# Optimization experiments

Hardware: AMD Instinct MI355X
Metric: run time of the kernel (lower is better)

The kernel has to match this reference:

```python
import jax, jax.numpy as jnp
import numpy as np

DIM = 128
HEADS = 4
DIM_HEAD = 32
HIDDEN = HEADS * DIM_HEAD  # 128
SCALE = DIM_HEAD ** -0.5


def setup_inputs() -> dict:
    key = jax.random.key(0)
    k1, k2, k3, k4 = jax.random.split(key, 4)
    b, c, h, w = 2, DIM, 64, 64
    x = jax.random.normal(k1, (b, c, h, w), dtype=jnp.float32)
    # conv1x1 weights stored as [out_ch, in_ch] (kernel is 1x1)
    w_qkv = jax.random.normal(k2, (3 * HIDDEN, DIM), dtype=jnp.float32) * (DIM ** -0.5)
    w_out = jax.random.normal(k3, (DIM, HIDDEN), dtype=jnp.float32) * (HIDDEN ** -0.5)
    b_out = jax.random.normal(k4, (DIM,), dtype=jnp.float32) * 0.01
    return {"x": x, "w_qkv": w_qkv, "w_out": w_out, "b_out": b_out}


def reference(x, w_qkv, w_out, b_out):
    b, c, h, w = x.shape
    n = h * w
    xf = x.reshape(b, c, n)                                   # [b,c,n]
    qkv = jnp.einsum('oc,bcn->bon', w_qkv, xf)                # conv1x1, no bias
    q, k, v = jnp.split(qkv, 3, axis=1)                       # each [b,hidden,n]
    q = q.reshape(b, HEADS, DIM_HEAD, n) * SCALE
    k = k.reshape(b, HEADS, DIM_HEAD, n)
    v = v.reshape(b, HEADS, DIM_HEAD, n)
    sim = jnp.einsum('bhdi,bhdj->bhij', q, k)                 # [b,h,n,n]
    attn = jax.nn.softmax(sim, axis=-1)
    out = jnp.einsum('bhij,bhdj->bhdi', attn, v)              # [b,h,d,n]
    out = out.reshape(b, HIDDEN, n)
    out = jnp.einsum('oc,bcn->bon', w_out, out) + b_out[None, :, None]
    return out.reshape(b, c, h, w) + x
```

## Files before the change

### kernel.cpp

```cpp
#include <hip/hip_runtime.h>
#include <hip/hip_bf16.h>

typedef __hip_bfloat16 bf16;
typedef float    f32x16 __attribute__((ext_vector_type(16)));
typedef __bf16   bf16x8 __attribute__((ext_vector_type(8)));
typedef unsigned uint4v __attribute__((ext_vector_type(4)));
typedef int      i32x2  __attribute__((ext_vector_type(2)));

#define N_TOK 4096
#define SCALE_L2E 0.2550348952703927f

__device__ __forceinline__ bf16x8 ld8(const bf16* p) { return *(const bf16x8*)p; }
__device__ __forceinline__ unsigned pack2(float a, float b) {
    unsigned short ua = __builtin_bit_cast(unsigned short, (__bf16)a);
    unsigned short ub = __builtin_bit_cast(unsigned short, (__bf16)b);
    return (unsigned)ua | ((unsigned)ub << 16);
}
__device__ __forceinline__ unsigned short f2b(float f) {
    return __builtin_bit_cast(unsigned short, (__bf16)f);
}
__device__ __forceinline__ __bf16 us2bf(unsigned short u) {
    return __builtin_bit_cast(__bf16, u);
}

__global__ void wconv(const float* __restrict__ wqkv, const float* __restrict__ wout,
                      bf16* __restrict__ wq, bf16* __restrict__ wo) {
    int idx = blockIdx.x * 256 + threadIdx.x;
    if (idx < 384 * 128) {
        float sc = (idx < 128 * 128) ? SCALE_L2E : 1.0f;
        ((unsigned short*)wq)[idx] = f2b(wqkv[idx] * sc);
    } else {
        int j = idx - 384 * 128;
        ((unsigned short*)wo)[j] = f2b(wout[j]);
    }
}

__global__ void __launch_bounds__(256)
qkv_mfma(const float* __restrict__ x, const bf16* __restrict__ wq,
         bf16* __restrict__ qt, bf16* __restrict__ kt, bf16* __restrict__ vt) {
    int tok0 = blockIdx.x * 64;
    int b    = blockIdx.y;
    int z    = blockIdx.z;
    __shared__ unsigned short xs[128 * 64];
    {
        int c = threadIdx.x >> 1, half = threadIdx.x & 1;
        const float4* x4 = (const float4*)(x + (size_t)(b * 128 + c) * N_TOK + tok0 + half * 32);
        unsigned* dst = (unsigned*)&xs[c * 64 + half * 32];
#pragma unroll
        for (int k = 0; k < 8; ++k) {
            float4 v4 = x4[k];
            dst[2 * k]     = pack2(v4.x, v4.y);
            dst[2 * k + 1] = pack2(v4.z, v4.w);
        }
    }
    __syncthreads();
    int lane = threadIdx.x & 63, wv = threadIdx.x >> 6;
    int tc = wv & 1, oh = wv >> 1;
    int ot = z * 2 + oh;
    int o0 = ot * 32;
    int i = lane & 31, hl = lane >> 5;

    bf16x8 xf[8], wf[8];
#pragma unroll
    for (int kb = 0; kb < 8; ++kb) {
        bf16x8 f;
#pragma unroll
        for (int e = 0; e < 8; ++e) f[e] = us2bf(xs[(kb * 16 + hl * 8 + e) * 64 + tc * 32 + i]);
        xf[kb] = f;
        wf[kb] = ld8(wq + (size_t)(o0 + i) * 128 + kb * 16 + hl * 8);
    }

    f32x16 D;
#pragma unroll
    for (int r = 0; r < 16; ++r) D[r] = 0.f;

    if (ot < 8) {
#pragma unroll
        for (int kb = 0; kb < 8; ++kb)
            D = __builtin_amdgcn_mfma_f32_32x32x16_bf16(xf[kb], wf[kb], D, 0, 0, 0);
        bf16* base = (ot < 4) ? qt : kt;
        int h = ot & 3;
        unsigned short* dst = (unsigned short*)(base +
            ((size_t)(b * 4 + h) * N_TOK + tok0 + tc * 32) * 32);
#pragma unroll
        for (int r = 0; r < 16; ++r) {
            int tr = (r & 3) + 8 * (r >> 2) + 4 * hl;
            dst[tr * 32 + i] = f2b(D[r]);
        }
    } else {
#pragma unroll
        for (int kb = 0; kb < 8; ++kb)
            D = __builtin_amdgcn_mfma_f32_32x32x16_bf16(wf[kb], xf[kb], D, 0, 0, 0);
        int h = ot - 8;
        unsigned short* dst = (unsigned short*)(vt +
            (size_t)(b * 4 + h) * (32 * N_TOK) + tok0 + tc * 32);
#pragma unroll
        for (int r = 0; r < 16; ++r) {
            int dr = (r & 3) + 8 * (r >> 2) + 4 * hl;
            dst[(size_t)dr * N_TOK + i] = f2b(D[r]);
        }
    }
}

#define KROW 40
#define KBUF_SZ (128 * KROW * 2)
#define VBUF_OFF (2 * KBUF_SZ)
#define VBUF_SZ (32 * 128 * 2)

__global__ void __launch_bounds__(512)
attn_mfma(const bf16* __restrict__ qt, const bf16* __restrict__ kt,
          const bf16* __restrict__ vt, bf16* __restrict__ ao) {
    int bid = blockIdx.x;
    int bh  = bid & 7;
    int qg  = bid >> 3;
    int tid = threadIdx.x;
    int lane = tid & 63, wv = tid >> 6;
    int qp = wv >> 2;
    int ks = wv & 3;
    int i = lane & 31, hl = lane >> 5;

    __shared__ char lds[2 * KBUF_SZ + 2 * VBUF_SZ];

    const bf16* qb = qt + (size_t)bh * (N_TOK * 32) + (size_t)(qg * 128 + qp * 64) * 32;
    bf16x8 q1a = ld8(qb + i * 32 + hl * 8);
    bf16x8 q2a = ld8(qb + i * 32 + 16 + hl * 8);
    bf16x8 q1b = ld8(qb + (32 + i) * 32 + hl * 8);
    bf16x8 q2b = ld8(qb + (32 + i) * 32 + 16 + hl * 8);

    int u = tid;
    const bf16* ksrc = kt + (size_t)bh * (N_TOK * 32) + (u >> 2) * 32 + (u & 3) * 8;
    const bf16* vsrc = vt + (size_t)bh * (32 * N_TOK) + (size_t)(u >> 4) * N_TOK + (u & 15) * 8;
    int kdst = (u >> 2) * 80 + (u & 3) * 16;
    int vdst = VBUF_OFF + (((u >> 4) * 256 + (u & 15) * 16) ^ (((u >> 4) & 7) << 4));

    int koff1 = (ks * 32 + i) * 80 + hl * 16;
    int koff2 = koff1 + 32;
    int voff1 = VBUF_OFF + ((i * 256 + ks * 64 + hl * 16) ^ ((i & 7) << 4));
    int voff2 = VBUF_OFF + ((i * 256 + ks * 64 + 32 + hl * 16) ^ ((i & 7) << 4));

    f32x16 OA, OB, Z;
#pragma unroll
    for (int r = 0; r < 16; ++r) { OA[r] = 0.f; OB[r] = 0.f; Z[r] = 0.f; }
    float lA = 0.f, lB = 0.f;

    *(uint4v*)(lds + kdst) = *(const uint4v*)ksrc;
    *(uint4v*)(lds + vdst) = *(const uint4v*)vsrc;
    __syncthreads();

    for (int t = 0; t < 32; ++t) {
        int cur = t & 1;
        uint4v nk, nv;
        if (t < 31) {
            nk = *(const uint4v*)(ksrc + (size_t)(t + 1) * 128 * 32);
            nv = *(const uint4v*)(vsrc + (t + 1) * 128);
        }
        bf16x8 ka1 = __builtin_bit_cast(bf16x8, *(const uint4v*)(lds + cur * KBUF_SZ + koff1));
        bf16x8 ka2 = __builtin_bit_cast(bf16x8, *(const uint4v*)(lds + cur * KBUF_SZ + koff2));
        bf16x8 va1 = __builtin_bit_cast(bf16x8, *(const uint4v*)(lds + cur * VBUF_SZ + voff1));
        bf16x8 va2 = __builtin_bit_cast(bf16x8, *(const uint4v*)(lds + cur * VBUF_SZ + voff2));

        f32x16 SA = __builtin_amdgcn_mfma_f32_32x32x16_bf16(ka1, q1a, Z, 0, 0, 0);
        SA = __builtin_amdgcn_mfma_f32_32x32x16_bf16(ka2, q2a, SA, 0, 0, 0);
        f32x16 SB = __builtin_amdgcn_mfma_f32_32x32x16_bf16(ka1, q1b, Z, 0, 0, 0);
        SB = __builtin_amdgcn_mfma_f32_32x32x16_bf16(ka2, q2b, SB, 0, 0, 0);

        float pA[16], pB[16];
#pragma unroll
        for (int r = 0; r < 16; ++r) { pA[r] = __builtin_amdgcn_exp2f(SA[r]); }
#pragma unroll
        for (int r = 0; r < 16; ++r) { pB[r] = __builtin_amdgcn_exp2f(SB[r]); }
#pragma unroll
        for (int r = 0; r < 16; ++r) { lA += pA[r]; lB += pB[r]; }

        {
            unsigned k0 = pack2(pA[0], pA[1]),   k1 = pack2(pA[2], pA[3]);
            unsigned k2 = pack2(pA[4], pA[5]),   k3 = pack2(pA[6], pA[7]);
            unsigned k4 = pack2(pA[8], pA[9]),   k5 = pack2(pA[10], pA[11]);
            unsigned k6 = pack2(pA[12], pA[13]), k7 = pack2(pA[14], pA[15]);
            i32x2 t1 = __builtin_amdgcn_permlane32_swap((int)k0, (int)k2, false, false);
            i32x2 t2 = __builtin_amdgcn_permlane32_swap((int)k1, (int)k3, false, false);
            i32x2 t3 = __builtin_amdgcn_permlane32_swap((int)k4, (int)k6, false, false);
            i32x2 t4 = __builtin_amdgcn_permlane32_swap((int)k5, (int)k7, false, false);
            uint4v B1u = {(unsigned)t1.x, (unsigned)t2.x, (unsigned)t1.y, (unsigned)t2.y};
            uint4v B2u = {(unsigned)t3.x, (unsigned)t4.x, (unsigned)t3.y, (unsigned)t4.y};
            OA = __builtin_amdgcn_mfma_f32_32x32x16_bf16(va1, __builtin_bit_cast(bf16x8, B1u), OA, 0, 0, 0);
            OA = __builtin_amdgcn_mfma_f32_32x32x16_bf16(va2, __builtin_bit_cast(bf16x8, B2u), OA, 0, 0, 0);
        }
        {
            unsigned k0 = pack2(pB[0], pB[1]),   k1 = pack2(pB[2], pB[3]);
            unsigned k2 = pack2(pB[4], pB[5]),   k3 = pack2(pB[6], pB[7]);
            unsigned k4 = pack2(pB[8], pB[9]),   k5 = pack2(pB[10], pB[11]);
            unsigned k6 = pack2(pB[12], pB[13]), k7 = pack2(pB[14], pB[15]);
            i32x2 t1 = __builtin_amdgcn_permlane32_swap((int)k0, (int)k2, false, false);
            i32x2 t2 = __builtin_amdgcn_permlane32_swap((int)k1, (int)k3, false, false);
            i32x2 t3 = __builtin_amdgcn_permlane32_swap((int)k4, (int)k6, false, false);
            i32x2 t4 = __builtin_amdgcn_permlane32_swap((int)k5, (int)k7, false, false);
            uint4v B1u = {(unsigned)t1.x, (unsigned)t2.x, (unsigned)t1.y, (unsigned)t2.y};
            uint4v B2u = {(unsigned)t3.x, (unsigned)t4.x, (unsigned)t3.y, (unsigned)t4.y};
            OB = __builtin_amdgcn_mfma_f32_32x32x16_bf16(va1, __builtin_bit_cast(bf16x8, B1u), OB, 0, 0, 0);
            OB = __builtin_amdgcn_mfma_f32_32x32x16_bf16(va2, __builtin_bit_cast(bf16x8, B2u), OB, 0, 0, 0);
        }

        if (t < 31) {
            int nxt = cur ^ 1;
            *(uint4v*)(lds + nxt * KBUF_SZ + kdst) = nk;
            *(uint4v*)(lds + nxt * VBUF_SZ + vdst) = nv;
        }
        __syncthreads();
    }

    lA += __shfl_xor(lA, 32);
    lB += __shfl_xor(lB, 32);
    float* fb = (float*)lds;
    float* ls = (float*)(lds + 24576);
    unsigned short* aop = (unsigned short*)(ao + (size_t)bh * (32 * N_TOK) + qg * 128 + qp * 64);

#pragma unroll
    for (int qtl = 0; qtl < 2; ++qtl) {
        const f32x16& O = qtl ? OB : OA;
        float l = qtl ? lB : lA;
        if (ks) {
            int s = qp * 3 + ks - 1;
#pragma unroll
            for (int r = 0; r < 16; ++r) fb[(s * 16 + r) * 64 + lane] = O[r];
            ls[s * 64 + lane] = l;
        }
        __syncthreads();
        if (ks == 0) {
            int s0 = qp * 3;
            float lt = l + ls[s0 * 64 + lane] + ls[(s0 + 1) * 64 + lane] + ls[(s0 + 2) * 64 + lane];
            float inv = 1.f / lt;
#pragma unroll
            for (int r = 0; r < 16; ++r) {
                float sv = O[r] + fb[((s0) * 16 + r) * 64 + lane] +
                           fb[((s0 + 1) * 16 + r) * 64 + lane] +
                           fb[((s0 + 2) * 16 + r) * 64 + lane];
                int d = (r & 3) + 8 * (r >> 2) + 4 * hl;
                aop[(size_t)d * N_TOK + qtl * 32 + i] = f2b(sv * inv);
            }
        }
        __syncthreads();
    }
}

__global__ void __launch_bounds__(256)
out_mfma(const bf16* __restrict__ ao, const bf16* __restrict__ wo,
         const float* __restrict__ bias, const float* __restrict__ x,
         float* __restrict__ out) {
    int tok0 = blockIdx.x * 64;
    int b    = blockIdx.y;
    int z    = blockIdx.z;
    __shared__ unsigned short as_[128 * 64];
    {
        int c = threadIdx.x >> 1, half = threadIdx.x & 1;
        const uint4v* src = (const uint4v*)(ao + (size_t)(b * 128 + c) * N_TOK + tok0 + half * 32);
        uint4v* dst = (uint4v*)&as_[c * 64 + half * 32];
#pragma unroll
        for (int k = 0; k < 4; ++k) dst[k] = src[k];
    }
    __syncthreads();
    int lane = threadIdx.x & 63, wv = threadIdx.x >> 6;
    int tc = wv & 1, oh = wv >> 1;
    int o0 = (z * 2 + oh) * 32;
    int i = lane & 31, hl = lane >> 5;

    bf16x8 af[8], wf[8];
#pragma unroll
    for (int kb = 0; kb < 8; ++kb) {
        bf16x8 f;
#pragma unroll
        for (int e = 0; e < 8; ++e) f[e] = us2bf(as_[(kb * 16 + hl * 8 + e) * 64 + tc * 32 + i]);
        af[kb] = f;
        wf[kb] = ld8(wo + (size_t)(o0 + i) * 128 + kb * 16 + hl * 8);
    }

    f32x16 D;
#pragma unroll
    for (int r = 0; r < 16; ++r) D[r] = 0.f;
#pragma unroll
    for (int kb = 0; kb < 8; ++kb)
        D = __builtin_amdgcn_mfma_f32_32x32x16_bf16(wf[kb], af[kb], D, 0, 0, 0);

#pragma unroll
    for (int r = 0; r < 16; ++r) {
        int o_r = o0 + (r & 3) + 8 * (r >> 2) + 4 * hl;
        size_t idx = ((size_t)b * 128 + o_r) * N_TOK + tok0 + tc * 32 + i;
        out[idx] = D[r] + bias[o_r] + x[idx];
    }
}

extern "C" void kernel_launch(void* const* d_in, const int* in_sizes, int n_in,
                              void* d_out, int out_size, void* d_ws, size_t ws_size,
                              hipStream_t stream) {
    const float* x     = (const float*)d_in[0];
    const float* w_qkv = (const float*)d_in[1];
    const float* w_out = (const float*)d_in[2];
    const float* b_out = (const float*)d_in[3];
    float* out = (float*)d_out;

    bf16* qt = (bf16*)d_ws;
    bf16* kt = qt + (size_t)8 * N_TOK * 32;
    bf16* vt = kt + (size_t)8 * N_TOK * 32;
    bf16* ao = vt + (size_t)8 * N_TOK * 32;
    bf16* wq = ao + (size_t)2 * 128 * N_TOK;
    bf16* wo = wq + (size_t)384 * 128;

    wconv    <<<dim3(256), 256, 0, stream>>>(w_qkv, w_out, wq, wo);
    qkv_mfma <<<dim3(64, 2, 6), 256, 0, stream>>>(x, wq, qt, kt, vt);
    attn_mfma<<<dim3(256), 512, 0, stream>>>(qt, kt, vt, ao);
    out_mfma <<<dim3(64, 2, 2), 256, 0, stream>>>(ao, wo, b_out, x, out);
}
```

Measured before the change: 112.3 us.

## Restructure projection tiling and LDS layouts for vectorized fragment loads

The QKV and output projection kernels now use 32-token blocks in which each block computes all output channels. This removes the redundant re-staging of x across the z grid dimension. Activations are staged into LDS token-major with an XOR swizzle, so MFMA fragments load as single 16-byte reads instead of eight scalar LDS loads. The attention kernel's K/V LDS tiles are also relaid into a flat fragment-ordered layout with no padding or swizzle. The cost is strided scalar global reads of x and ao during staging, and possible bank conflicts in the new attention layout.

Measured after the change: 113.9 us. Within noise of the previous version (+1.4%).

```diff
diff --git a/kernel.cpp b/kernel.cpp
--- a/kernel.cpp
+++ b/kernel.cpp
@@ -18,9 +18,6 @@
 }
 __device__ __forceinline__ unsigned short f2b(float f) {
     return __builtin_bit_cast(unsigned short, (__bf16)f);
-}
-__device__ __forceinline__ __bf16 us2bf(unsigned short u) {
-    return __builtin_bit_cast(__bf16, u);
 }
 
 __global__ void wconv(const float* __restrict__ wqkv, const float* __restrict__ wout,
@@ -38,62 +35,57 @@
 __global__ void __launch_bounds__(256)
 qkv_mfma(const float* __restrict__ x, const bf16* __restrict__ wq,
          bf16* __restrict__ qt, bf16* __restrict__ kt, bf16* __restrict__ vt) {
-    int tok0 = blockIdx.x * 64;
+    int tok0 = blockIdx.x * 32;
     int b    = blockIdx.y;
-    int z    = blockIdx.z;
-    __shared__ unsigned short xs[128 * 64];
+    __shared__ char xs[32 * 256];
     {
-        int c = threadIdx.x >> 1, half = threadIdx.x & 1;
-        const float4* x4 = (const float4*)(x + (size_t)(b * 128 + c) * N_TOK + tok0 + half * 32);
-        unsigned* dst = (unsigned*)&xs[c * 64 + half * 32];
-#pragma unroll
-        for (int k = 0; k < 8; ++k) {
-            float4 v4 = x4[k];
-            dst[2 * k]     = pack2(v4.x, v4.y);
-            dst[2 * k + 1] = pack2(v4.z, v4.w);
-        }
+        int tok = threadIdx.x & 31, cg = threadIdx.x >> 5;
+        const float* xp = x + ((size_t)b * 128 + cg * 16) * N_TOK + tok0 + tok;
+        unsigned u[8];
+#pragma unroll
+        for (int j = 0; j < 8; ++j)
+            u[j] = pack2(xp[(size_t)(2 * j) * N_TOK], xp[(size_t)(2 * j + 1) * N_TOK]);
+        int base = tok * 256, sw = (tok & 7) << 4;
+        *(uint4v*)(xs + base + ((cg * 32) ^ sw))      = (uint4v){u[0], u[1], u[2], u[3]};
+        *(uint4v*)(xs + base + ((cg * 32 + 16) ^ sw)) = (uint4v){u[4], u[5], u[6], u[7]};
     }
     __syncthreads();
     int lane = threadIdx.x & 63, wv = threadIdx.x >> 6;
-    int tc = wv & 1, oh = wv >> 1;
-    int ot = z * 2 + oh;
-    int o0 = ot * 32;
     int i = lane & 31, hl = lane >> 5;
 
-    bf16x8 xf[8], wf[8];
-#pragma unroll
-    for (int kb = 0; kb < 8; ++kb) {
-        bf16x8 f;
-#pragma unroll
-        for (int e = 0; e < 8; ++e) f[e] = us2bf(xs[(kb * 16 + hl * 8 + e) * 64 + tc * 32 + i]);
-        xf[kb] = f;
-        wf[kb] = ld8(wq + (size_t)(o0 + i) * 128 + kb * 16 + hl * 8);
-    }
-
-    f32x16 D;
-#pragma unroll
-    for (int r = 0; r < 16; ++r) D[r] = 0.f;
-
-    if (ot < 8) {
+    bf16x8 xf[8];
+#pragma unroll
+    for (int kb = 0; kb < 8; ++kb)
+        xf[kb] = __builtin_bit_cast(bf16x8,
+            *(const uint4v*)(xs + i * 256 + ((kb * 32 + hl * 16) ^ ((i & 7) << 4))));
+
+#pragma unroll
+    for (int qk = 0; qk < 2; ++qk) {
+        int o0 = qk * 128 + wv * 32;
+        const bf16* wrow = wq + (size_t)(o0 + i) * 128 + hl * 8;
+        f32x16 D;
+#pragma unroll
+        for (int r = 0; r < 16; ++r) D[r] = 0.f;
 #pragma unroll
         for (int kb = 0; kb < 8; ++kb)
-            D = __builtin_amdgcn_mfma_f32_32x32x16_bf16(xf[kb], wf[kb], D, 0, 0, 0);
-        bf16* base = (ot < 4) ? qt : kt;
-        int h = ot & 3;
-        unsigned short* dst = (unsigned short*)(base +
-            ((size_t)(b * 4 + h) * N_TOK + tok0 + tc * 32) * 32);
+            D = __builtin_amdgcn_mfma_f32_32x32x16_bf16(xf[kb], ld8(wrow + kb * 16), D, 0, 0, 0);
+        bf16* base = qk ? kt : qt;
+        unsigned short* dst = (unsigned short*)(base + ((size_t)(b * 4 + wv) * N_TOK + tok0) * 32);
 #pragma unroll
         for (int r = 0; r < 16; ++r) {
             int tr = (r & 3) + 8 * (r >> 2) + 4 * hl;
             dst[tr * 32 + i] = f2b(D[r]);
         }
-    } else {
+    }
+    {
+        const bf16* wrow = wq + (size_t)(256 + wv * 32 + i) * 128 + hl * 8;
+        f32x16 D;
+#pragma unroll
+        for (int r = 0; r < 16; ++r) D[r] = 0.f;
 #pragma unroll
         for (int kb = 0; kb < 8; ++kb)
-            D = __builtin_amdgcn_mfma_f32_32x32x16_bf16(wf[kb], xf[kb], D, 0, 0, 0);
-        int h = ot - 8;
-        unsigned short* dst = (unsigned short*)(vt +
-            (size_t)(b * 4 + h) * (32 * N_TOK) + tok0 + tc * 32);
+            D = __builtin_amdgcn_mfma_f32_32x32x16_bf16(ld8(wrow + kb * 16), xf[kb], D, 0, 0, 0);
+        unsigned short* dst = (unsigned short*)(vt + (size_t)(b * 4 + wv) * (32 * N_TOK) + tok0);
 #pragma unroll
         for (int r = 0; r < 16; ++r) {
             int dr = (r & 3) + 8 * (r >> 2) + 4 * hl;
@@ -102,10 +94,8 @@
     }
 }
 
-#define KROW 40
-#define KBUF_SZ (128 * KROW * 2)
-#define VBUF_OFF (2 * KBUF_SZ)
-#define VBUF_SZ (32 * 128 * 2)
+#define BUF_SZ 16384
+#define VOFF   8192
 
 __global__ void __launch_bounds__(512)
 attn_mfma(const bf16* __restrict__ qt, const bf16* __restrict__ kt,
@@ -119,7 +109,7 @@
     int ks = wv & 3;
     int i = lane & 31, hl = lane >> 5;
 
-    __shared__ char lds[2 * KBUF_SZ + 2 * VBUF_SZ];
+    __shared__ char lds[2 * BUF_SZ];
 
     const bf16* qb = qt + (size_t)bh * (N_TOK * 32) + (size_t)(qg * 128 + qp * 64) * 32;
     bf16x8 q1a = ld8(qb + i * 32 + hl * 8);
@@ -128,15 +118,15 @@
     bf16x8 q2b = ld8(qb + (32 + i) * 32 + 16 + hl * 8);
 
     int u = tid;
-    const bf16* ksrc = kt + (size_t)bh * (N_TOK * 32) + (u >> 2) * 32 + (u & 3) * 8;
-    const bf16* vsrc = vt + (size_t)bh * (32 * N_TOK) + (size_t)(u >> 4) * N_TOK + (u & 15) * 8;
-    int kdst = (u >> 2) * 80 + (u & 3) * 16;
-    int vdst = VBUF_OFF + (((u >> 4) * 256 + (u & 15) * 16) ^ (((u >> 4) & 7) << 4));
-
-    int koff1 = (ks * 32 + i) * 80 + hl * 16;
-    int koff2 = koff1 + 32;
-    int voff1 = VBUF_OFF + ((i * 256 + ks * 64 + hl * 16) ^ ((i & 7) << 4));
-    int voff2 = VBUF_OFF + ((i * 256 + ks * 64 + 32 + hl * 16) ^ ((i & 7) << 4));
+    const bf16* ksrc = kt + (size_t)bh * (N_TOK * 32) + (u & 127) * 32 + (u >> 7) * 8;
+    int kdst = u * 16;
+    const bf16* vsrc = vt + (size_t)bh * (32 * N_TOK) + (size_t)(u & 31) * N_TOK + (u >> 5) * 8;
+    int vdst = VOFF + ((u >> 5) * 32 + (u & 31)) * 16;
+
+    int koff1 = (hl * 128 + ks * 32 + i) * 16;
+    int koff2 = koff1 + 4096;
+    int voff1 = VOFF + ((ks * 4 + hl) * 32 + i) * 16;
+    int voff2 = voff1 + 1024;
 
     f32x16 OA, OB, Z;
 #pragma unroll
@@ -154,10 +144,11 @@
             nk = *(const uint4v*)(ksrc + (size_t)(t + 1) * 128 * 32);
             nv = *(const uint4v*)(vsrc + (t + 1) * 128);
         }
-        bf16x8 ka1 = __builtin_bit_cast(bf16x8, *(const uint4v*)(lds + cur * KBUF_SZ + koff1));
-        bf16x8 ka2 = __builtin_bit_cast(bf16x8, *(const uint4v*)(lds + cur * KBUF_SZ + koff2));
-        bf16x8 va1 = __builtin_bit_cast(bf16x8, *(const uint4v*)(lds + cur * VBUF_SZ + voff1));
-        bf16x8 va2 = __builtin_bit_cast(bf16x8, *(const uint4v*)(lds + cur * VBUF_SZ + voff2));
+        const char* B = lds + cur * BUF_SZ;
+        bf16x8 ka1 = __builtin_bit_cast(bf16x8, *(const uint4v*)(B + koff1));
+        bf16x8 ka2 = __builtin_bit_cast(bf16x8, *(const uint4v*)(B + koff2));
+        bf16x8 va1 = __builtin_bit_cast(bf16x8, *(const uint4v*)(B + voff1));
+        bf16x8 va2 = __builtin_bit_cast(bf16x8, *(const uint4v*)(B + voff2));
 
         f32x16 SA = __builtin_amdgcn_mfma_f32_32x32x16_bf16(ka1, q1a, Z, 0, 0, 0);
         SA = __builtin_amdgcn_mfma_f32_32x32x16_bf16(ka2, q2a, SA, 0, 0, 0);
@@ -202,9 +193,9 @@
         }
 
         if (t < 31) {
-            int nxt = cur ^ 1;
-            *(uint4v*)(lds + nxt * KBUF_SZ + kdst) = nk;
-            *(uint4v*)(lds + nxt * VBUF_SZ + vdst) = nv;
+            char* NB = lds + (cur ^ 1) * BUF_SZ;
+            *(uint4v*)(NB + kdst) = nk;
+            *(uint4v*)(NB + vdst) = nv;
         }
         __syncthreads();
     }
@@ -247,44 +238,42 @@
 out_mfma(const bf16* __restrict__ ao, const bf16* __restrict__ wo,
          const float* __restrict__ bias, const float* __restrict__ x,
          float* __restrict__ out) {
-    int tok0 = blockIdx.x * 64;
+    int tok0 = blockIdx.x * 32;
     int b    = blockIdx.y;
-    int z    = blockIdx.z;
-    __shared__ unsigned short as_[128 * 64];
+    __shared__ char as[32 * 256];
     {
-        int c = threadIdx.x >> 1, half = threadIdx.x & 1;
-        const uint4v* src = (const uint4v*)(ao + (size_t)(b * 128 + c) * N_TOK + tok0 + half * 32);
-        uint4v* dst = (uint4v*)&as_[c * 64 + half * 32];
-#pragma unroll
-        for (int k = 0; k < 4; ++k) dst[k] = src[k];
+        int tok = threadIdx.x & 31, cg = threadIdx.x >> 5;
+        const unsigned short* ap = (const unsigned short*)ao +
+            ((size_t)b * 128 + cg * 16) * N_TOK + tok0 + tok;
+        unsigned u[8];
+#pragma unroll
+        for (int j = 0; j < 8; ++j)
+            u[j] = (unsigned)ap[(size_t)(2 * j) * N_TOK] |
+                   ((unsigned)ap[(size_t)(2 * j + 1) * N_TOK] << 16);
+        int base = tok * 256, sw = (tok & 7) << 4;
+        *(uint4v*)(as + base + ((cg * 32) ^ sw))      = (uint4v){u[0], u[1], u[2], u[3]};
+        *(uint4v*)(as + base + ((cg * 32 + 16) ^ sw)) = (uint4v){u[4], u[5], u[6], u[7]};
     }
     __syncthreads();
     int lane = threadIdx.x & 63, wv = threadIdx.x >> 6;
-    int tc = wv & 1, oh = wv >> 1;
-    int o0 = (z * 2 + oh) * 32;
     int i = lane & 31, hl = lane >> 5;
-
-    bf16x8 af[8], wf[8];
+    int o0 = wv * 32;
+
+    f32x16 D;
+#pragma unroll
+    for (int r = 0; r < 16; ++r) D[r] = 0.f;
+    const bf16* wrow = wo + (size_t)(o0 + i) * 128 + hl * 8;
 #pragma unroll
     for (int kb = 0; kb < 8; ++kb) {
-        bf16x8 f;
-#pragma unroll
-        for (int e = 0; e < 8; ++e) f[e] = us2bf(as_[(kb * 16 + hl * 8 + e) * 64 + tc * 32 + i]);
-        af[kb] = f;
-        wf[kb] = ld8(wo + (size_t)(o0 + i) * 128 + kb * 16 + hl * 8);
-    }
-
-    f32x16 D;
-#pragma unroll
-    for (int r = 0; r < 16; ++r) D[r] = 0.f;
-#pragma unroll
-    for (int kb = 0; kb < 8; ++kb)
-        D = __builtin_amdgcn_mfma_f32_32x32x16_bf16(wf[kb], af[kb], D, 0, 0, 0);
+        bf16x8 af = __builtin_bit_cast(bf16x8,
+            *(const uint4v*)(as + i * 256 + ((kb * 32 + hl * 16) ^ ((i & 7) << 4))));
+        D = __builtin_amdgcn_mfma_f32_32x32x16_bf16(ld8(wrow + kb * 16), af, D, 0, 0, 0);
+    }
 
 #pragma unroll
     for (int r = 0; r < 16; ++r) {
         int o_r = o0 + (r & 3) + 8 * (r >> 2) + 4 * hl;
-        size_t idx = ((size_t)b * 128 + o_r) * N_TOK + tok0 + tc * 32 + i;
+        size_t idx = ((size_t)b * 128 + o_r) * N_TOK + tok0 + i;
         out[idx] = D[r] + bias[o_r] + x[idx];
     }
 }
@@ -306,7 +295,7 @@
     bf16* wo = wq + (size_t)384 * 128;
 
     wconv    <<<dim3(256), 256, 0, stream>>>(w_qkv, w_out, wq, wo);
-    qkv_mfma <<<dim3(64, 2, 6), 256, 0, stream>>>(x, wq, qt, kt, vt);
+    qkv_mfma <<<dim3(128, 2), 256, 0, stream>>>(x, wq, qt, kt, vt);
     attn_mfma<<<dim3(256), 512, 0, stream>>>(qt, kt, vt, ao);
-    out_mfma <<<dim3(64, 2, 2), 256, 0, stream>>>(ao, wo, b_out, x, out);
-}
+    out_mfma <<<dim3(128, 2), 256, 0, stream>>>(ao, wo, b_out, x, out);
+}
```
